# Optimization experiments

Measured on AMD Instinct MI355X. Metric: run time of the kernel, lower is better.

The kernel has to match this reference:

```python
import jax, jax.numpy as jnp
import numpy as np

B, SEQ, DIM, D, K = 32, 2048, 512, 512, 128


def _ln(x, g, b, eps=1e-5):
    m = x.mean(-1, keepdims=True)
    v = ((x - m) ** 2).mean(-1, keepdims=True)
    return (x - m) / jnp.sqrt(v + eps) * g + b


def _gelu(v):
    return jax.nn.gelu(v, approximate=False)


def _diff_topk(s, k, t):
    # s: (B, N) scores; iterative relaxed top-k (Xie & Ermon style).
    def step(carry, _):
        a = jax.nn.softmax(carry / t, axis=-1)
        carry = carry + jnp.log(jnp.clip(1.0 - a, 1e-6, 1.0))
        return carry, a
    _, Ws = jax.lax.scan(step, s, None, length=k)  # (k, B, N)
    return jnp.transpose(Ws, (1, 0, 2))            # (B, k, N)


def setup_inputs():
    key = jax.random.key(0)
    ks = jax.random.split(key, 6)
    w = lambda k_, shape: jax.random.normal(k_, shape, dtype=jnp.float32) * 0.02
    return {
        'x': jax.random.normal(ks[0], (B, SEQ, DIM), dtype=jnp.float32),
        'tau': jnp.array(0.0, dtype=jnp.float32),
        'ln1_g': jnp.ones((DIM,), jnp.float32), 'ln1_b': jnp.zeros((DIM,), jnp.float32),
        'W1': w(ks[1], (DIM, D)), 'b1': jnp.zeros((D,), jnp.float32),
        'ln2_g': jnp.ones((SEQ,), jnp.float32), 'ln2_b': jnp.zeros((SEQ,), jnp.float32),
        'W2': w(ks[2], (SEQ, SEQ)), 'b2': jnp.zeros((SEQ,), jnp.float32),
        'ln3_g': jnp.ones((D,), jnp.float32), 'ln3_b': jnp.zeros((D,), jnp.float32),
        'W3': w(ks[3], (D, D + 1)), 'b3': jnp.zeros((D + 1,), jnp.float32),
        'ln4_g': jnp.ones((D,), jnp.float32), 'ln4_b': jnp.zeros((D,), jnp.float32),
        'W4': w(ks[4], (D, DIM)), 'b4': jnp.zeros((DIM,), jnp.float32),
    }


def reference(x, tau, ln1_g, ln1_b, W1, b1, ln2_g, ln2_b, W2, b2,
              ln3_g, ln3_b, W3, b3, ln4_g, ln4_b, W4, b4):
    # tok_proj: LN(dim) -> Linear(dim, D) -> GELU
    x_tok = _gelu(_ln(x, ln1_g, ln1_b) @ W1 + b1)                  # (B, N, D)
    # ch_proj over the token axis: LN(seq) -> Linear(seq, seq) -> GELU
    xt = jnp.swapaxes(x_tok, 1, 2)                                  # (B, D, N)
    x_ch = jnp.swapaxes(_gelu(_ln(xt, ln2_g, ln2_b) @ W2 + b2), 1, 2)
    # proj -> split score | features
    h = _ln(x_tok + x_ch, ln3_g, ln3_b) @ W3 + b3                   # (B, N, D+1)
    x_score, x_proj = h[..., 0], h[..., 1:]
    t = jax.nn.sigmoid(jnp.clip(tau, -2.0, 5.0))
    Wmat = _diff_topk(x_score, K, t)                                # (B, k, N)
    Z = jnp.einsum('bkn,bnd->bkd', Wmat, x_proj)                    # soft gather
    Y = jnp.einsum('bkn,bkd->bnd', Wmat, Z)                         # soft scatter
    return _ln(x_proj + Y, ln4_g, ln4_b) @ W4 + b4                  # (B, N, dim)
```

## Files before the change

### kernel.cpp

```cpp
#include <hip/hip_runtime.h>
#include <math.h>

#define B_   32
#define SEQ_ 2048
#define DIM_ 512
#define KSEL 128

typedef _Float16 f16;
typedef _Float16 half8 __attribute__((ext_vector_type(8)));
typedef float floatx4 __attribute__((ext_vector_type(4)));

#define LSTR2 32

__device__ __forceinline__ float gelu_exact(float v) {
  return 0.5f * v * (1.0f + erff(v * 0.70710678118654752440f));
}

__global__ __launch_bounds__(256) void rowstats512(const float* __restrict__ X,
                                                   float* __restrict__ mean,
                                                   float* __restrict__ rstd) {
  int row = blockIdx.x * 4 + (threadIdx.x >> 6);
  int l = threadIdx.x & 63;
  const float4* p = (const float4*)(X + (size_t)row * 512);
  float4 v0 = p[l * 2], v1 = p[l * 2 + 1];
  float s = v0.x + v0.y + v0.z + v0.w + v1.x + v1.y + v1.z + v1.w;
  float q = v0.x*v0.x + v0.y*v0.y + v0.z*v0.z + v0.w*v0.w
          + v1.x*v1.x + v1.y*v1.y + v1.z*v1.z + v1.w*v1.w;
#pragma unroll
  for (int off = 32; off > 0; off >>= 1) {
    s += __shfl_down(s, off);
    q += __shfl_down(q, off);
  }
  if (l == 0) {
    float m = s * (1.0f / 512.0f);
    float var = q * (1.0f / 512.0f) - m * m;
    mean[row] = m;
    rstd[row] = rsqrtf(var + 1e-5f);
  }
}

__global__ __launch_bounds__(256) void rowstats512_f16(const f16* __restrict__ X,
                                                       float* __restrict__ mean,
                                                       float* __restrict__ rstd) {
  int row = blockIdx.x * 4 + (threadIdx.x >> 6);
  int l = threadIdx.x & 63;
  half8 h = *(const half8*)(X + (size_t)row * 512 + l * 8);
  float s = 0.f, q = 0.f;
#pragma unroll
  for (int i = 0; i < 8; ++i) { float v = (float)h[i]; s += v; q += v * v; }
#pragma unroll
  for (int off = 32; off > 0; off >>= 1) {
    s += __shfl_down(s, off);
    q += __shfl_down(q, off);
  }
  if (l == 0) {
    float m = s * (1.0f / 512.0f);
    float var = q * (1.0f / 512.0f) - m * m;
    mean[row] = m;
    rstd[row] = rsqrtf(var + 1e-5f);
  }
}

__global__ __launch_bounds__(512) void colstats_part(const f16* __restrict__ xtok,
                                                     float2* __restrict__ part) {
  int b = blockIdx.x >> 3, pr = blockIdx.x & 7;
  int d = threadIdx.x;
  const f16* src = xtok + ((size_t)b * SEQ_ + (size_t)pr * 256) * 512 + d;
  float s = 0.f, q = 0.f;
#pragma unroll 4
  for (int i = 0; i < 256; ++i) {
    float v = (float)src[(size_t)i * 512];
    s += v; q += v * v;
  }
  part[(size_t)blockIdx.x * 512 + d] = make_float2(s, q);
}

__global__ __launch_bounds__(256) void colstats_fin(const float2* __restrict__ part,
                                                    float* __restrict__ mean,
                                                    float* __restrict__ rstd) {
  int idx = blockIdx.x * 256 + threadIdx.x;
  int b = idx >> 9;
  float s = 0.f, q = 0.f;
#pragma unroll
  for (int p = 0; p < 8; ++p) {
    float2 v = part[((size_t)(b * 8 + p)) * 512 + (idx & 511)];
    s += v.x; q += v.y;
  }
  float m = s * (1.0f / 2048.0f);
  mean[idx] = m;
  rstd[idx] = rsqrtf(q * (1.0f / 2048.0f) - m * m + 1e-5f);
}

template <typename T>
__global__ __launch_bounds__(256) void transpose_cvt(const T* __restrict__ src,
                                                     f16* __restrict__ dst,
                                                     int R, int C, long sb, long db) {
  __shared__ float tile[32][33];
  const T* s = src + (long)blockIdx.z * sb;
  f16* d = dst + (long)blockIdx.z * db;
  int c0 = blockIdx.x * 32, r0 = blockIdx.y * 32;
  int tx = threadIdx.x, ty = threadIdx.y;
#pragma unroll
  for (int i = 0; i < 4; ++i) {
    int r = r0 + ty + i * 8, c = c0 + tx;
    if (r < R && c < C) tile[ty + i * 8][tx] = (float)s[(long)r * C + c];
  }
  __syncthreads();
#pragma unroll
  for (int i = 0; i < 4; ++i) {
    int c = c0 + ty + i * 8, r = r0 + tx;
    if (c < C && r < R) d[(long)c * R + r] = (f16)tile[tx][ty + i * 8];
  }
}

__global__ __launch_bounds__(256) void trans2_kernel(const f16* __restrict__ xtok,
    const float* __restrict__ mean2, const float* __restrict__ rstd2,
    const float* __restrict__ g2, const float* __restrict__ bl2,
    f16* __restrict__ A2) {
  __shared__ float tile[32][33];
  int b = blockIdx.z;
  const f16* src = xtok + (long)b * SEQ_ * 512;
  f16* dst = A2 + (long)b * 512 * SEQ_;
  int d0 = blockIdx.x * 32, s0 = blockIdx.y * 32;
  int tx = threadIdx.x, ty = threadIdx.y;
  float m = mean2[b * 512 + d0 + tx];
  float rs = rstd2[b * 512 + d0 + tx];
#pragma unroll
  for (int i = 0; i < 4; ++i) {
    int s = s0 + ty + i * 8;
    float v = (float)src[(long)s * 512 + d0 + tx];
    tile[ty + i * 8][tx] = (v - m) * rs * g2[s] + bl2[s];
  }
  __syncthreads();
#pragma unroll
  for (int i = 0; i < 4; ++i) {
    int d = d0 + ty + i * 8, s = s0 + tx;
    dst[(long)d * SEQ_ + s] = (f16)tile[tx][ty + i * 8];
  }
}


__device__ __forceinline__ void stage_gll(const f16* __restrict__ src, long ld,
                                          int row0, int k0, f16* S, int t) {
  int w = t >> 6, lane = t & 63;
  int r = lane >> 2, c8 = (lane & 3) * 8;
#pragma unroll
  for (int i = 0; i < 2; ++i) {
    int chunk = w * 2 + i;
    const f16* g = src + (long)(row0 + chunk * 16 + r) * ld + k0 + c8;
    f16* l = S + chunk * 16 * LSTR2;
    __builtin_amdgcn_global_load_lds(
        (const __attribute__((address_space(1))) void*)g,
        (__attribute__((address_space(3))) void*)l, 16, 0, 0);
  }
}

__device__ __forceinline__ void stage_a_ln_f32(const float* __restrict__ src, long ld,
    const float* __restrict__ mean, const float* __restrict__ rstd,
    const float* __restrict__ g, const float* __restrict__ bl,
    int row0, int k0, f16* S, int t) {
  int row = t >> 1, kc = (t & 1) * 16;
  int r = row0 + row, c = k0 + kc;
  float m = mean[r], sd = rstd[r];
  const float* p = src + (long)r * ld + c;
  float v[16], gv[16], bv[16];
#pragma unroll
  for (int i = 0; i < 4; ++i) {
    float4 q = ((const float4*)p)[i];
    v[i*4+0]=q.x; v[i*4+1]=q.y; v[i*4+2]=q.z; v[i*4+3]=q.w;
    float4 gq = ((const float4*)(g + c))[i];
    gv[i*4+0]=gq.x; gv[i*4+1]=gq.y; gv[i*4+2]=gq.z; gv[i*4+3]=gq.w;
    float4 bq = ((const float4*)(bl + c))[i];
    bv[i*4+0]=bq.x; bv[i*4+1]=bq.y; bv[i*4+2]=bq.z; bv[i*4+3]=bq.w;
  }
  half8 o0, o1;
#pragma unroll
  for (int i = 0; i < 8; ++i) {
    o0[i] = (f16)((v[i] - m) * sd * gv[i] + bv[i]);
    o1[i] = (f16)((v[i + 8] - m) * sd * gv[i + 8] + bv[i + 8]);
  }
  *(half8*)(S + row * LSTR2 + kc) = o0;
  *(half8*)(S + row * LSTR2 + kc + 8) = o1;
}

__device__ __forceinline__ void stage_a_ln_f16(const f16* __restrict__ src, long ld,
    const float* __restrict__ mean, const float* __restrict__ rstd,
    const float* __restrict__ g, const float* __restrict__ bl,
    int row0, int k0, f16* S, int t) {
  int row = t >> 1, kc = (t & 1) * 16;
  int r = row0 + row, c = k0 + kc;
  float m = mean[r], sd = rstd[r];
  const f16* p = src + (long)r * ld + c;
  half8 h0 = *(const half8*)(p);
  half8 h1 = *(const half8*)(p + 8);
  float gv[16], bv[16];
#pragma unroll
  for (int i = 0; i < 4; ++i) {
    float4 gq = ((const float4*)(g + c))[i];
    gv[i*4+0]=gq.x; gv[i*4+1]=gq.y; gv[i*4+2]=gq.z; gv[i*4+3]=gq.w;
    float4 bq = ((const float4*)(bl + c))[i];
    bv[i*4+0]=bq.x; bv[i*4+1]=bq.y; bv[i*4+2]=bq.z; bv[i*4+3]=bq.w;
  }
  half8 o0, o1;
#pragma unroll
  for (int i = 0; i < 8; ++i) {
    o0[i] = (f16)(((float)h0[i] - m) * sd * gv[i] + bv[i]);
    o1[i] = (f16)(((float)h1[i] - m) * sd * gv[i + 8] + bv[i + 8]);
  }
  *(half8*)(S + row * LSTR2 + kc) = o0;
  *(half8*)(S + row * LSTR2 + kc + 8) = o1;
}

__device__ __forceinline__ void mfma_step(const f16* As, const f16* Bs, int lane,
                                          int wr, int wc, floatx4 acc[4][4]) {
  int kc = (lane >> 4) * 8;
  int rl = lane & 15;
  half8 a[4], b[4];
#pragma unroll
  for (int mi = 0; mi < 4; ++mi)
    a[mi] = *(const half8*)(As + (wr * 64 + mi * 16 + rl) * LSTR2 + kc);
#pragma unroll
  for (int ni = 0; ni < 4; ++ni)
    b[ni] = *(const half8*)(Bs + (wc * 64 + ni * 16 + rl) * LSTR2 + kc);
#pragma unroll
  for (int mi = 0; mi < 4; ++mi)
#pragma unroll
    for (int ni = 0; ni < 4; ++ni)
      acc[mi][ni] = __builtin_amdgcn_mfma_f32_16x16x32_f16(a[mi], b[ni], acc[mi][ni], 0, 0, 0);
}

#define GEMM_PROLOG \
  __shared__ __attribute__((aligned(16))) f16 As[128 * LSTR2]; \
  __shared__ __attribute__((aligned(16))) f16 Bs[128 * LSTR2]; \
  int t = threadIdx.x; \
  int lane = t & 63, w = t >> 6, wr = w >> 1, wc = w & 1; \
  floatx4 acc[4][4]; \
  _Pragma("unroll") for (int mi = 0; mi < 4; ++mi) \
  _Pragma("unroll") for (int ni = 0; ni < 4; ++ni) acc[mi][ni] = (floatx4){0.f,0.f,0.f,0.f};

__global__ __launch_bounds__(256) void g1_kernel(const float* __restrict__ x,
    const float* __restrict__ mean, const float* __restrict__ rstd,
    const float* __restrict__ g1, const float* __restrict__ bl1,
    const f16* __restrict__ W1T, const float* __restrict__ b1,
    f16* __restrict__ xtok) {
  GEMM_PROLOG
  int m0 = blockIdx.y * 128, n0 = blockIdx.x * 128;
  for (int k0 = 0; k0 < 512; k0 += 32) {
    stage_a_ln_f32(x, 512, mean, rstd, g1, bl1, m0, k0, As, t);
    stage_gll(W1T, 512, n0, k0, Bs, t);
    __syncthreads();
    mfma_step(As, Bs, lane, wr, wc, acc);
    __syncthreads();
  }
#pragma unroll
  for (int mi = 0; mi < 4; ++mi)
#pragma unroll
    for (int ni = 0; ni < 4; ++ni) {
      int c = n0 + wc * 64 + ni * 16 + (lane & 15);
      float bias = b1[c];
      int r0 = m0 + wr * 64 + mi * 16 + (lane >> 4) * 4;
#pragma unroll
      for (int j = 0; j < 4; ++j)
        xtok[(long)(r0 + j) * 512 + c] = (f16)gelu_exact(acc[mi][ni][j] + bias);
    }
}

__global__ __launch_bounds__(256) void g2_kernel(const f16* __restrict__ W2T,
    const f16* __restrict__ A2, const float* __restrict__ b2,
    const f16* __restrict__ xtok, f16* __restrict__ xsum) {
  GEMM_PROLOG
  int b = blockIdx.z;
  int m0 = blockIdx.y * 128, n0 = blockIdx.x * 128;
  const f16* A2b = A2 + (long)b * 512 * SEQ_;
  const f16* xtb = xtok + (long)b * SEQ_ * 512;
  f16* xsb = xsum + (long)b * SEQ_ * 512;
  for (int k0 = 0; k0 < SEQ_; k0 += 32) {
    stage_gll(W2T, SEQ_, m0, k0, As, t);
    stage_gll(A2b, SEQ_, n0, k0, Bs, t);
    __syncthreads();
    mfma_step(As, Bs, lane, wr, wc, acc);
    __syncthreads();
  }
#pragma unroll
  for (int mi = 0; mi < 4; ++mi)
#pragma unroll
    for (int ni = 0; ni < 4; ++ni) {
      int c = n0 + wc * 64 + ni * 16 + (lane & 15);
      int r0 = m0 + wr * 64 + mi * 16 + (lane >> 4) * 4;
#pragma unroll
      for (int j = 0; j < 4; ++j) {
        int r = r0 + j;
        long idx = (long)r * 512 + c;
        float v = gelu_exact(acc[mi][ni][j] + b2[r]);
        xsb[idx] = (f16)((float)xtb[idx] + v);
      }
    }
}

__global__ __launch_bounds__(256) void g3_kernel(const f16* __restrict__ xsum,
    const float* __restrict__ mean, const float* __restrict__ rstd,
    const float* __restrict__ g3, const float* __restrict__ bl3,
    const f16* __restrict__ BT , const float* __restrict__ b3,
    f16* __restrict__ xproj) {
  GEMM_PROLOG
  int m0 = blockIdx.y * 128, n0 = blockIdx.x * 128;
  for (int k0 = 0; k0 < 512; k0 += 32) {
    stage_a_ln_f16(xsum, 512, mean, rstd, g3, bl3, m0, k0, As, t);
    stage_gll(BT, 512, n0, k0, Bs, t);
    __syncthreads();
    mfma_step(As, Bs, lane, wr, wc, acc);
    __syncthreads();
  }
#pragma unroll
  for (int mi = 0; mi < 4; ++mi)
#pragma unroll
    for (int ni = 0; ni < 4; ++ni) {
      int c = n0 + wc * 64 + ni * 16 + (lane & 15);
      float bias = b3[c + 1];
      int r0 = m0 + wr * 64 + mi * 16 + (lane >> 4) * 4;
#pragma unroll
      for (int j = 0; j < 4; ++j)
        xproj[(long)(r0 + j) * 512 + c] = (f16)(acc[mi][ni][j] + bias);
    }
}

__global__ __launch_bounds__(256) void score_kernel(const f16* __restrict__ xsum,
    const float* __restrict__ mean, const float* __restrict__ rstd,
    const float* __restrict__ g3, const float* __restrict__ bl3,
    const f16* __restrict__ w3c , const float* __restrict__ b3,
    float* __restrict__ xscore) {
  int row = blockIdx.x * 4 + (threadIdx.x >> 6);
  int l = threadIdx.x & 63;
  float m = mean[row], sd = rstd[row];
  half8 h = *(const half8*)(xsum + (long)row * 512 + l * 8);
  half8 wv = *(const half8*)(w3c + l * 8);
  float acc = 0.f;
#pragma unroll
  for (int i = 0; i < 8; ++i) {
    int d = l * 8 + i;
    float v = ((float)h[i] - m) * sd * g3[d] + bl3[d];
    acc += v * (float)wv[i];
  }
#pragma unroll
  for (int off = 32; off > 0; off >>= 1) acc += __shfl_down(acc, off);
  if (l == 0) xscore[row] = acc + b3[0];
}

__global__ __launch_bounds__(256) void topk_kernel(const float* __restrict__ xscore,
                                                   const float* __restrict__ tau,
                                                   f16* __restrict__ Wm) {
  int b = blockIdx.x, t = threadIdx.x;
  __shared__ float red[4];
  float tv = fminf(fmaxf(tau[0], -2.0f), 5.0f);
  float temp = 1.0f / (1.0f + expf(-tv));
  float it = 1.0f / temp;
  float c[8];
  const float* xs = xscore + (size_t)b * SEQ_;
#pragma unroll
  for (int i = 0; i < 8; ++i) c[i] = xs[t * 8 + i];
  for (int k = 0; k < KSEL; ++k) {
    float e[8];
    float p = 0.f;
#pragma unroll
    for (int i = 0; i < 8; ++i) { e[i] = expf(c[i] * it); p += e[i]; }
#pragma unroll
    for (int off = 32; off > 0; off >>= 1) p += __shfl_down(p, off);
    if ((t & 63) == 0) red[t >> 6] = p;
    __syncthreads();
    float S = red[0] + red[1] + red[2] + red[3];
    float iS = 1.0f / S;
    float a[8];
    half8 h;
#pragma unroll
    for (int i = 0; i < 8; ++i) { a[i] = e[i] * iS; h[i] = (f16)a[i]; }
    *(half8*)(Wm + ((size_t)b * KSEL + k) * SEQ_ + t * 8) = h;
#pragma unroll
    for (int i = 0; i < 8; ++i) c[i] += logf(fmaxf(1.0f - a[i], 1e-6f));
    __syncthreads();
  }
}

__global__ __launch_bounds__(256) void gz_kernel(const f16* __restrict__ Wm,
    const f16* __restrict__ xprojT, float* __restrict__ Zpart) {
  GEMM_PROLOG
  int b = blockIdx.z, kc = blockIdx.y;
  int n0 = blockIdx.x * 128;
  const f16* A = Wm + (long)b * KSEL * SEQ_;
  const f16* BT = xprojT + (long)b * 512 * SEQ_;
  float* Zb = Zpart + ((long)b * 2 + kc) * KSEL * 512;
  int kbeg = kc * 1024, kend = kbeg + 1024;
  for (int k0 = kbeg; k0 < kend; k0 += 32) {
    stage_gll(A, SEQ_, 0, k0, As, t);
    stage_gll(BT, SEQ_, n0, k0, Bs, t);
    __syncthreads();
    mfma_step(As, Bs, lane, wr, wc, acc);
    __syncthreads();
  }
#pragma unroll
  for (int mi = 0; mi < 4; ++mi)
#pragma unroll
    for (int ni = 0; ni < 4; ++ni) {
      int c = n0 + wc * 64 + ni * 16 + (lane & 15);
      int r0 = wr * 64 + mi * 16 + (lane >> 4) * 4;
#pragma unroll
      for (int j = 0; j < 4; ++j)
        Zb[(long)(r0 + j) * 512 + c] = acc[mi][ni][j];
    }
}

__global__ __launch_bounds__(256) void ztrans_kernel(const float* __restrict__ Zpart,
                                                     f16* __restrict__ ZT) {
  __shared__ float tile[32][33];
  int b = blockIdx.z;
  int c0 = blockIdx.x * 32, r0 = blockIdx.y * 32;
  int tx = threadIdx.x, ty = threadIdx.y;
  const float* p0 = Zpart + ((long)b * 2 + 0) * KSEL * 512;
  const float* p1 = Zpart + ((long)b * 2 + 1) * KSEL * 512;
#pragma unroll
  for (int i = 0; i < 4; ++i) {
    int r = r0 + ty + i * 8, c = c0 + tx;
    tile[ty + i * 8][tx] = p0[(long)r * 512 + c] + p1[(long)r * 512 + c];
  }
  __syncthreads();
  f16* d = ZT + (long)b * 512 * KSEL;
#pragma unroll
  for (int i = 0; i < 4; ++i) {
    int c = c0 + ty + i * 8, r = r0 + tx;
    d[(long)c * KSEL + r] = (f16)tile[tx][ty + i * 8];
  }
}

__global__ __launch_bounds__(256) void gy_kernel(const f16* __restrict__ WmT,
    const f16* __restrict__ ZT, const f16* __restrict__ xproj,
    f16* __restrict__ rbuf) {
  GEMM_PROLOG
  int b = blockIdx.z;
  int m0 = blockIdx.y * 128, n0 = blockIdx.x * 128;
  const f16* A = WmT + (long)b * SEQ_ * KSEL;
  const f16* BT = ZT + (long)b * 512 * KSEL;
  const f16* xpb = xproj + (long)b * SEQ_ * 512;
  f16* rb = rbuf + (long)b * SEQ_ * 512;
  for (int k0 = 0; k0 < KSEL; k0 += 32) {
    stage_gll(A, KSEL, m0, k0, As, t);
    stage_gll(BT, KSEL, n0, k0, Bs, t);
    __syncthreads();
    mfma_step(As, Bs, lane, wr, wc, acc);
    __syncthreads();
  }
#pragma unroll
  for (int mi = 0; mi < 4; ++mi)
#pragma unroll
    for (int ni = 0; ni < 4; ++ni) {
      int c = n0 + wc * 64 + ni * 16 + (lane & 15);
      int r0 = m0 + wr * 64 + mi * 16 + (lane >> 4) * 4;
#pragma unroll
      for (int j = 0; j < 4; ++j) {
        long idx = (long)(r0 + j) * 512 + c;
        rb[idx] = (f16)((float)xpb[idx] + acc[mi][ni][j]);
      }
    }
}

__global__ __launch_bounds__(256) void g4_kernel(const f16* __restrict__ rbuf,
    const float* __restrict__ mean, const float* __restrict__ rstd,
    const float* __restrict__ g4, const float* __restrict__ bl4,
    const f16* __restrict__ W4T, const float* __restrict__ b4,
    float* __restrict__ out) {
  GEMM_PROLOG
  int m0 = blockIdx.y * 128, n0 = blockIdx.x * 128;
  for (int k0 = 0; k0 < 512; k0 += 32) {
    stage_a_ln_f16(rbuf, 512, mean, rstd, g4, bl4, m0, k0, As, t);
    stage_gll(W4T, 512, n0, k0, Bs, t);
    __syncthreads();
    mfma_step(As, Bs, lane, wr, wc, acc);
    __syncthreads();
  }
#pragma unroll
  for (int mi = 0; mi < 4; ++mi)
#pragma unroll
    for (int ni = 0; ni < 4; ++ni) {
      int c = n0 + wc * 64 + ni * 16 + (lane & 15);
      float bias = b4[c];
      int r0 = m0 + wr * 64 + mi * 16 + (lane >> 4) * 4;
#pragma unroll
      for (int j = 0; j < 4; ++j)
        out[(long)(r0 + j) * 512 + c] = acc[mi][ni][j] + bias;
    }
}

extern "C" void kernel_launch(void* const* d_in, const int* in_sizes, int n_in,
                              void* d_out, int out_size, void* d_ws, size_t ws_size,
                              hipStream_t stream) {
  const float* x    = (const float*)d_in[0];
  const float* tau  = (const float*)d_in[1];
  const float* g1   = (const float*)d_in[2];
  const float* bl1  = (const float*)d_in[3];
  const float* W1   = (const float*)d_in[4];
  const float* b1   = (const float*)d_in[5];
  const float* g2   = (const float*)d_in[6];
  const float* bl2  = (const float*)d_in[7];
  const float* W2   = (const float*)d_in[8];
  const float* b2   = (const float*)d_in[9];
  const float* g3   = (const float*)d_in[10];
  const float* bl3  = (const float*)d_in[11];
  const float* W3   = (const float*)d_in[12];
  const float* b3   = (const float*)d_in[13];
  const float* g4   = (const float*)d_in[14];
  const float* bl4  = (const float*)d_in[15];
  const float* W4   = (const float*)d_in[16];
  const float* b4   = (const float*)d_in[17];
  float* out = (float*)d_out;

  const long NTOK = (long)B_ * SEQ_;

  char* ws = (char*)d_ws;
  f16* regA   = (f16*)(ws);
  f16* regB   = (f16*)(ws + (64l << 20));
  float* Zpart = (float*)(ws + (128l << 20));
  f16* W2T    = (f16*)(ws + (144l << 20));
  f16* W1T    = (f16*)(ws + (152l << 20));
  f16* W3T    = (f16*)(ws + (153l << 20));
  f16* W4T    = (f16*)(ws + (154l << 20));
  float* xscore = (float*)(ws + (155l << 20));
  float* meanA  = (float*)(ws + (156l << 20));
  float* rstdA  = meanA + NTOK;
  float* mean2  = rstdA + NTOK;
  float* rstd2  = mean2 + B_ * 512;
  float2* part  = (float2*)(rstd2 + B_ * 512);

  f16* xtok   = (f16*)d_out;
  f16* xprojT = (f16*)d_out;
  f16* Wm     = (f16*)((char*)d_out + (64l << 20));
  f16* WmT    = (f16*)((char*)d_out + (80l << 20));
  f16* ZT     = (f16*)((char*)d_out + (96l << 20));

  f16* A2    = regA;
  f16* xsum  = regB;
  f16* xproj = regA;
  f16* rbuf  = regB;

  dim3 tb(32, 8);

  transpose_cvt<float><<<dim3(16, 16, 1), tb, 0, stream>>>(W1, W1T, 512, 512, 0, 0);
  transpose_cvt<float><<<dim3(64, 64, 1), tb, 0, stream>>>(W2, W2T, 2048, 2048, 0, 0);
  transpose_cvt<float><<<dim3(17, 16, 1), tb, 0, stream>>>(W3, W3T, 512, 513, 0, 0);
  transpose_cvt<float><<<dim3(16, 16, 1), tb, 0, stream>>>(W4, W4T, 512, 512, 0, 0);

  rowstats512<<<NTOK / 4, 256, 0, stream>>>(x, meanA, rstdA);
  g1_kernel<<<dim3(4, 512), 256, 0, stream>>>(x, meanA, rstdA, g1, bl1, W1T, b1, xtok);

  colstats_part<<<B_ * 8, 512, 0, stream>>>(xtok, part);
  colstats_fin<<<64, 256, 0, stream>>>(part, mean2, rstd2);
  trans2_kernel<<<dim3(16, 64, B_), tb, 0, stream>>>(xtok, mean2, rstd2, g2, bl2, A2);
  g2_kernel<<<dim3(4, 16, B_), 256, 0, stream>>>(W2T, A2, b2, xtok, xsum);

  rowstats512_f16<<<NTOK / 4, 256, 0, stream>>>(xsum, meanA, rstdA);
  score_kernel<<<NTOK / 4, 256, 0, stream>>>(xsum, meanA, rstdA, g3, bl3, W3T, b3, xscore);
  g3_kernel<<<dim3(4, 512), 256, 0, stream>>>(xsum, meanA, rstdA, g3, bl3, W3T + 512, b3, xproj);

  topk_kernel<<<B_, 256, 0, stream>>>(xscore, tau, Wm);

  transpose_cvt<f16><<<dim3(16, 64, B_), tb, 0, stream>>>(xproj, xprojT, 2048, 512,
      (long)SEQ_ * 512, (long)512 * SEQ_);
  transpose_cvt<f16><<<dim3(64, 4, B_), tb, 0, stream>>>(Wm, WmT, 128, 2048,
      (long)KSEL * SEQ_, (long)SEQ_ * KSEL);

  gz_kernel<<<dim3(4, 2, B_), 256, 0, stream>>>(Wm, xprojT, Zpart);
  ztrans_kernel<<<dim3(16, 4, B_), tb, 0, stream>>>(Zpart, ZT);

  gy_kernel<<<dim3(4, 16, B_), 256, 0, stream>>>(WmT, ZT, xproj, rbuf);

  rowstats512_f16<<<NTOK / 4, 256, 0, stream>>>(rbuf, meanA, rstdA);
  g4_kernel<<<dim3(4, 512), 256, 0, stream>>>(rbuf, meanA, rstdA, g4, bl4, W4T, b4, out);
}
```

Measured before the change: 878.3 us.

## Rewrite ch-proj GEMM with 256x256 double-buffered swizzled LDS tiles and 8 waves

Replaces the 128x128, K=32, single-buffered g2 GEMM with a 512-thread kernel. Each block computes a 256x256 output tile over K=64 steps. Global-to-LDS loads are double-buffered and interleaved with the MFMA phases, use an XOR-swizzled LDS layout to avoid bank conflicts, and raise wave priority with s_setprio around MFMA bursts. This aims to cut global traffic per FLOP and hide load latency in the dominant SEQxSEQ GEMM. In exchange, the kernel uses 128 KB of LDS and many accumulator registers, which limits occupancy. The ZT buffer is also moved into the workspace.

```diff
diff --git a/kernel.cpp b/kernel.cpp
--- a/kernel.cpp
+++ b/kernel.cpp
@@ -139,7 +139,6 @@
   }
 }
 
-
 __device__ __forceinline__ void stage_gll(const f16* __restrict__ src, long ld,
                                           int row0, int k0, f16* S, int t) {
   int w = t >> 6, lane = t & 63;
@@ -265,36 +264,130 @@
     }
 }
 
-__global__ __launch_bounds__(256) void g2_kernel(const f16* __restrict__ W2T,
+__device__ __forceinline__ void stage_tile256(const f16* __restrict__ srcbase, long ld,
+                                              int k0, f16* dst, int tid) {
+  int w = tid >> 6, l = tid & 63;
+  int colh = ((l & 7) ^ (l >> 3)) << 3;
+  int rsub = w * 8 + (l >> 3);
+#pragma unroll
+  for (int q = 0; q < 4; ++q) {
+    const f16* g = srcbase + (long)(q * 64 + rsub) * ld + k0 + colh;
+    f16* lp = dst + (long)(q * 512 + w * 64) * 8;
+    __builtin_amdgcn_global_load_lds(
+        (const __attribute__((address_space(1))) void*)g,
+        (__attribute__((address_space(3))) void*)lp, 16, 0, 0);
+  }
+}
+
+__device__ __forceinline__ half8 frag_swz(const f16* buf, int row, int kslot, int rl) {
+  return *(const half8*)(buf + (long)row * 64 + (((kslot ^ (rl & 7))) << 3));
+}
+
+__global__ __launch_bounds__(512, 2) void g2_8p(const f16* __restrict__ W2T,
     const f16* __restrict__ A2, const float* __restrict__ b2,
     const f16* __restrict__ xtok, f16* __restrict__ xsum) {
-  GEMM_PROLOG
+  __shared__ __attribute__((aligned(16))) f16 Abuf[2][256 * 64];
+  __shared__ __attribute__((aligned(16))) f16 Bbuf[2][256 * 64];
+  int tid = threadIdx.x;
+  int l = tid & 63, w = tid >> 6;
+  int wr = w >> 2, wc = w & 3;
+  int rl = l & 15, sl = l >> 4;
   int b = blockIdx.z;
-  int m0 = blockIdx.y * 128, n0 = blockIdx.x * 128;
-  const f16* A2b = A2 + (long)b * 512 * SEQ_;
+  int m0 = blockIdx.y * 256;
+  int n0 = blockIdx.x * 256;
+  const f16* Am = W2T + (long)m0 * SEQ_;
+  const f16* Bm = A2 + (long)b * 512 * SEQ_ + (long)n0 * SEQ_;
   const f16* xtb = xtok + (long)b * SEQ_ * 512;
   f16* xsb = xsum + (long)b * SEQ_ * 512;
-  for (int k0 = 0; k0 < SEQ_; k0 += 32) {
-    stage_gll(W2T, SEQ_, m0, k0, As, t);
-    stage_gll(A2b, SEQ_, n0, k0, Bs, t);
-    __syncthreads();
-    mfma_step(As, Bs, lane, wr, wc, acc);
-    __syncthreads();
-  }
-#pragma unroll
-  for (int mi = 0; mi < 4; ++mi)
-#pragma unroll
-    for (int ni = 0; ni < 4; ++ni) {
-      int c = n0 + wc * 64 + ni * 16 + (lane & 15);
-      int r0 = m0 + wr * 64 + mi * 16 + (lane >> 4) * 4;
-#pragma unroll
-      for (int j = 0; j < 4; ++j) {
-        int r = r0 + j;
-        long idx = (long)r * 512 + c;
-        float v = gelu_exact(acc[mi][ni][j] + b2[r]);
-        xsb[idx] = (f16)((float)xtb[idx] + v);
+
+  floatx4 acc[8][4];
+#pragma unroll
+  for (int mf = 0; mf < 8; ++mf)
+#pragma unroll
+    for (int nf = 0; nf < 4; ++nf) acc[mf][nf] = (floatx4){0.f, 0.f, 0.f, 0.f};
+
+  const int NT = SEQ_ / 64;
+  stage_tile256(Am, SEQ_, 0, Abuf[0], tid);
+  stage_tile256(Bm, SEQ_, 0, Bbuf[0], tid);
+  __syncthreads();
+
+  for (int t = 0; t < NT; ++t) {
+    int c = t & 1;
+    const f16* Ab = Abuf[c];
+    const f16* Bb = Bbuf[c];
+    half8 afr[4], bfr[4];
+
+    if (t + 1 < NT) stage_tile256(Am, SEQ_, (t + 1) * 64, Abuf[c ^ 1], tid);
+#pragma unroll
+    for (int nf = 0; nf < 4; ++nf) bfr[nf] = frag_swz(Bb, wc * 64 + nf * 16 + rl, sl, rl);
+#pragma unroll
+    for (int mf = 0; mf < 4; ++mf) afr[mf] = frag_swz(Ab, wr * 128 + mf * 16 + rl, sl, rl);
+    __builtin_amdgcn_s_barrier();
+    __builtin_amdgcn_s_setprio(1);
+#pragma unroll
+    for (int mf = 0; mf < 4; ++mf)
+#pragma unroll
+      for (int nf = 0; nf < 4; ++nf)
+        acc[mf][nf] = __builtin_amdgcn_mfma_f32_16x16x32_f16(afr[mf], bfr[nf], acc[mf][nf], 0, 0, 0);
+    __builtin_amdgcn_s_setprio(0);
+    __builtin_amdgcn_s_barrier();
+
+    if (t + 1 < NT) stage_tile256(Bm, SEQ_, (t + 1) * 64, Bbuf[c ^ 1], tid);
+#pragma unroll
+    for (int mf = 0; mf < 4; ++mf) afr[mf] = frag_swz(Ab, wr * 128 + (mf + 4) * 16 + rl, sl, rl);
+    __builtin_amdgcn_s_barrier();
+    __builtin_amdgcn_s_setprio(1);
+#pragma unroll
+    for (int mf = 0; mf < 4; ++mf)
+#pragma unroll
+      for (int nf = 0; nf < 4; ++nf)
+        acc[mf + 4][nf] = __builtin_amdgcn_mfma_f32_16x16x32_f16(afr[mf], bfr[nf], acc[mf + 4][nf], 0, 0, 0);
+    __builtin_amdgcn_s_setprio(0);
+    __builtin_amdgcn_s_barrier();
+
+#pragma unroll
+    for (int nf = 0; nf < 4; ++nf) bfr[nf] = frag_swz(Bb, wc * 64 + nf * 16 + rl, 4 + sl, rl);
+#pragma unroll
+    for (int mf = 0; mf < 4; ++mf) afr[mf] = frag_swz(Ab, wr * 128 + mf * 16 + rl, 4 + sl, rl);
+    __builtin_amdgcn_s_barrier();
+    __builtin_amdgcn_s_setprio(1);
+#pragma unroll
+    for (int mf = 0; mf < 4; ++mf)
+#pragma unroll
+      for (int nf = 0; nf < 4; ++nf)
+        acc[mf][nf] = __builtin_amdgcn_mfma_f32_16x16x32_f16(afr[mf], bfr[nf], acc[mf][nf], 0, 0, 0);
+    __builtin_amdgcn_s_setprio(0);
+    __builtin_amdgcn_s_barrier();
+
+#pragma unroll
+    for (int mf = 0; mf < 4; ++mf) afr[mf] = frag_swz(Ab, wr * 128 + (mf + 4) * 16 + rl, 4 + sl, rl);
+    __builtin_amdgcn_s_setprio(1);
+#pragma unroll
+    for (int mf = 0; mf < 4; ++mf)
+#pragma unroll
+      for (int nf = 0; nf < 4; ++nf)
+        acc[mf + 4][nf] = __builtin_amdgcn_mfma_f32_16x16x32_f16(afr[mf], bfr[nf], acc[mf + 4][nf], 0, 0, 0);
+    __builtin_amdgcn_s_setprio(0);
+
+    __syncthreads();
+  }
+
+#pragma unroll
+  for (int mf = 0; mf < 8; ++mf) {
+    int rbase = m0 + wr * 128 + mf * 16 + sl * 4;
+#pragma unroll
+    for (int j = 0; j < 4; ++j) {
+      int r = rbase + j;
+      float bias = b2[r];
+      long rowoff = (long)r * 512;
+#pragma unroll
+      for (int nf = 0; nf < 4; ++nf) {
+        int cc = n0 + wc * 64 + nf * 16 + rl;
+        float v = gelu_exact(acc[mf][nf][j] + bias);
+        xsb[rowoff + cc] = (f16)((float)xtb[rowoff + cc] + v);
       }
     }
+  }
 }
 
 __global__ __launch_bounds__(256) void g3_kernel(const f16* __restrict__ xsum,
@@ -327,7 +420,7 @@
 __global__ __launch_bounds__(256) void score_kernel(const f16* __restrict__ xsum,
     const float* __restrict__ mean, const float* __restrict__ rstd,
     const float* __restrict__ g3, const float* __restrict__ bl3,
-    const f16* __restrict__ w3c , const float* __restrict__ b3,
+    const f16* __restrict__ w3c, const float* __restrict__ b3,
     float* __restrict__ xscore) {
   int row = blockIdx.x * 4 + (threadIdx.x >> 6);
   int l = threadIdx.x & 63;
@@ -527,12 +620,12 @@
   float* mean2  = rstdA + NTOK;
   float* rstd2  = mean2 + B_ * 512;
   float2* part  = (float2*)(rstd2 + B_ * 512);
+  f16* ZT     = (f16*)(ws + (157l << 20));
 
   f16* xtok   = (f16*)d_out;
   f16* xprojT = (f16*)d_out;
   f16* Wm     = (f16*)((char*)d_out + (64l << 20));
   f16* WmT    = (f16*)((char*)d_out + (80l << 20));
-  f16* ZT     = (f16*)((char*)d_out + (96l << 20));
 
   f16* A2    = regA;
   f16* xsum  = regB;
@@ -552,7 +645,7 @@
   colstats_part<<<B_ * 8, 512, 0, stream>>>(xtok, part);
   colstats_fin<<<64, 256, 0, stream>>>(part, mean2, rstd2);
   trans2_kernel<<<dim3(16, 64, B_), tb, 0, stream>>>(xtok, mean2, rstd2, g2, bl2, A2);
-  g2_kernel<<<dim3(4, 16, B_), 256, 0, stream>>>(W2T, A2, b2, xtok, xsum);
+  g2_8p<<<dim3(2, 8, B_), 512, 0, stream>>>(W2T, A2, b2, xtok, xsum);
 
   rowstats512_f16<<<NTOK / 4, 256, 0, stream>>>(xsum, meanA, rstdA);
   score_kernel<<<NTOK / 4, 256, 0, stream>>>(xsum, meanA, rstdA, g3, bl3, W3T, b3, xscore);
```

After: 889.1 us, median of 3. No clear change (+1.2%).

## Replace g2 GEMM with 256x256-tile, 8-wave, double-buffered pipelined kernel

Applied to the files above, without the earlier changes.

Replaces the 128x128 single-buffered g2 GEMM with a 256x256 tile kernel using 512 threads (8 waves), a double-buffered LDS pipeline of async global_load_lds stages interleaved with MFMA phases, and an XOR swizzle to avoid LDS bank conflicts. The goal is to overlap memory loads with 16x16x32 MFMA compute and raise arithmetic intensity for the largest GEMM. It also moves the ZT buffer into the workspace. The cost is heavier register pressure (128 accumulator floats per thread), manual barriers and vmcnt waits that are fragile if the tile count or staging order is wrong.

```diff
diff --git a/kernel.cpp b/kernel.cpp
--- a/kernel.cpp
+++ b/kernel.cpp
@@ -139,7 +139,6 @@
   }
 }
 
-
 __device__ __forceinline__ void stage_gll(const f16* __restrict__ src, long ld,
                                           int row0, int k0, f16* S, int t) {
   int w = t >> 6, lane = t & 63;
@@ -265,36 +264,124 @@
     }
 }
 
-__global__ __launch_bounds__(256) void g2_kernel(const f16* __restrict__ W2T,
+
+__device__ __forceinline__ void stage_half(const f16* __restrict__ srcbase, long ld,
+                                           f16* dst, int tid) {
+#pragma unroll
+  for (int q = 0; q < 2; ++q) {
+    int row = q * 128 + (tid >> 2);
+    int slot = (tid & 3) ^ ((row >> 1) & 3);
+    const f16* g = srcbase + (long)row * ld + slot * 8;
+    f16* lp = dst + (long)(q * 128 + (tid >> 6) * 16) * 32;
+    __builtin_amdgcn_global_load_lds(
+        (const __attribute__((address_space(1))) void*)g,
+        (__attribute__((address_space(3))) void*)lp, 16, 0, 0);
+  }
+}
+
+__device__ __forceinline__ half8 frag32(const f16* buf, int row, int sl) {
+  return *(const half8*)(buf + (long)row * 32 + ((sl ^ ((row >> 1) & 3)) << 3));
+}
+
+#define ASM_BAR()      asm volatile("s_barrier" ::: "memory")
+#define ASM_WAITBAR4() asm volatile("s_waitcnt vmcnt(4)\ns_barrier" ::: "memory")
+
+__global__ __launch_bounds__(512, 2) void g2_8p(const f16* __restrict__ W2T,
     const f16* __restrict__ A2, const float* __restrict__ b2,
     const f16* __restrict__ xtok, f16* __restrict__ xsum) {
-  GEMM_PROLOG
+  __shared__ __attribute__((aligned(16))) f16 Ah[2][2][256 * 32];
+  __shared__ __attribute__((aligned(16))) f16 Bh[2][2][256 * 32];
+  int tid = threadIdx.x;
+  int l = tid & 63, w = tid >> 6;
+  int wr = w >> 2, wc = w & 3;
+  int rl = l & 15, sl = l >> 4;
   int b = blockIdx.z;
-  int m0 = blockIdx.y * 128, n0 = blockIdx.x * 128;
-  const f16* A2b = A2 + (long)b * 512 * SEQ_;
+  int m0 = blockIdx.y * 256;
+  int n0 = blockIdx.x * 256;
+  const f16* Am = W2T + (long)m0 * SEQ_;
+  const f16* Bm = A2 + (long)b * 512 * SEQ_ + (long)n0 * SEQ_;
   const f16* xtb = xtok + (long)b * SEQ_ * 512;
   f16* xsb = xsum + (long)b * SEQ_ * 512;
-  for (int k0 = 0; k0 < SEQ_; k0 += 32) {
-    stage_gll(W2T, SEQ_, m0, k0, As, t);
-    stage_gll(A2b, SEQ_, n0, k0, Bs, t);
-    __syncthreads();
-    mfma_step(As, Bs, lane, wr, wc, acc);
-    __syncthreads();
-  }
-#pragma unroll
-  for (int mi = 0; mi < 4; ++mi)
-#pragma unroll
-    for (int ni = 0; ni < 4; ++ni) {
-      int c = n0 + wc * 64 + ni * 16 + (lane & 15);
-      int r0 = m0 + wr * 64 + mi * 16 + (lane >> 4) * 4;
-#pragma unroll
-      for (int j = 0; j < 4; ++j) {
-        int r = r0 + j;
-        long idx = (long)r * 512 + c;
-        float v = gelu_exact(acc[mi][ni][j] + b2[r]);
-        xsb[idx] = (f16)((float)xtb[idx] + v);
+
+  floatx4 acc[8][4];
+#pragma unroll
+  for (int mf = 0; mf < 8; ++mf)
+#pragma unroll
+    for (int nf = 0; nf < 4; ++nf) acc[mf][nf] = (floatx4){0.f, 0.f, 0.f, 0.f};
+
+  half8 afr[4], bfr[4];
+
+#define STAGE(base, tile, kk, dstbuf) \
+  stage_half(base + (long)((tile) & 31) * 64 + (kk) * 32, SEQ_, dstbuf, tid)
+
+#define READ_B(d, kk) \
+  _Pragma("unroll") for (int nf = 0; nf < 4; ++nf) \
+    bfr[nf] = frag32(Bh[d][kk], wc * 64 + nf * 16 + rl, sl);
+
+#define READ_A(d, kk, mb) \
+  _Pragma("unroll") for (int mi = 0; mi < 4; ++mi) \
+    afr[mi] = frag32(Ah[d][kk], wr * 128 + ((mb) + mi) * 16 + rl, sl);
+
+#define MFMA16(mb) \
+  __builtin_amdgcn_s_setprio(1); \
+  _Pragma("unroll") for (int mi = 0; mi < 4; ++mi) \
+  _Pragma("unroll") for (int nf = 0; nf < 4; ++nf) \
+    acc[(mb) + mi][nf] = __builtin_amdgcn_mfma_f32_16x16x32_f16(afr[mi], bfr[nf], acc[(mb) + mi][nf], 0, 0, 0); \
+  __builtin_amdgcn_s_setprio(0);
+
+  STAGE(Am, 0, 0, Ah[0][0]); STAGE(Am, 0, 1, Ah[0][1]);
+  STAGE(Bm, 0, 0, Bh[0][0]); STAGE(Bm, 0, 1, Bh[0][1]);
+  STAGE(Am, 1, 0, Ah[1][0]); STAGE(Bm, 1, 0, Bh[1][0]);
+  asm volatile("s_waitcnt vmcnt(0)" ::: "memory");
+  __builtin_amdgcn_s_barrier();
+
+  for (int i = 0; i < 16; ++i) {
+    STAGE(Am, 2 * i + 1, 1, Ah[1][1]);
+    READ_B(0, 0); READ_A(0, 0, 0);
+    ASM_BAR(); MFMA16(0); ASM_BAR();
+    STAGE(Bm, 2 * i + 1, 1, Bh[1][1]);
+    READ_A(0, 0, 4);
+    ASM_BAR(); MFMA16(4); ASM_BAR();
+    STAGE(Am, 2 * i + 2, 0, Ah[0][0]);
+    READ_B(0, 1); READ_A(0, 1, 0);
+    ASM_BAR(); MFMA16(0); ASM_BAR();
+    STAGE(Bm, 2 * i + 2, 0, Bh[0][0]);
+    READ_A(0, 1, 4);
+    ASM_BAR(); MFMA16(4); ASM_WAITBAR4();
+    STAGE(Am, 2 * i + 2, 1, Ah[0][1]);
+    READ_B(1, 0); READ_A(1, 0, 0);
+    ASM_BAR(); MFMA16(0); ASM_BAR();
+    STAGE(Bm, 2 * i + 2, 1, Bh[0][1]);
+    READ_A(1, 0, 4);
+    ASM_BAR(); MFMA16(4); ASM_BAR();
+    STAGE(Am, 2 * i + 3, 0, Ah[1][0]);
+    READ_B(1, 1); READ_A(1, 1, 0);
+    ASM_BAR(); MFMA16(0); ASM_BAR();
+    STAGE(Bm, 2 * i + 3, 0, Bh[1][0]);
+    READ_A(1, 1, 4);
+    ASM_BAR(); MFMA16(4); ASM_WAITBAR4();
+  }
+
+#pragma unroll
+  for (int mf = 0; mf < 8; ++mf) {
+    int rbase = m0 + wr * 128 + mf * 16 + sl * 4;
+#pragma unroll
+    for (int j = 0; j < 4; ++j) {
+      int r = rbase + j;
+      float bias = b2[r];
+      long rowoff = (long)r * 512;
+#pragma unroll
+      for (int nf = 0; nf < 4; ++nf) {
+        int cc = n0 + wc * 64 + nf * 16 + rl;
+        float v = gelu_exact(acc[mf][nf][j] + bias);
+        xsb[rowoff + cc] = (f16)((float)xtb[rowoff + cc] + v);
       }
     }
+  }
+#undef STAGE
+#undef READ_B
+#undef READ_A
+#undef MFMA16
 }
 
 __global__ __launch_bounds__(256) void g3_kernel(const f16* __restrict__ xsum,
@@ -327,7 +414,7 @@
 __global__ __launch_bounds__(256) void score_kernel(const f16* __restrict__ xsum,
     const float* __restrict__ mean, const float* __restrict__ rstd,
     const float* __restrict__ g3, const float* __restrict__ bl3,
-    const f16* __restrict__ w3c , const float* __restrict__ b3,
+    const f16* __restrict__ w3c, const float* __restrict__ b3,
     float* __restrict__ xscore) {
   int row = blockIdx.x * 4 + (threadIdx.x >> 6);
   int l = threadIdx.x & 63;
@@ -527,12 +614,12 @@
   float* mean2  = rstdA + NTOK;
   float* rstd2  = mean2 + B_ * 512;
   float2* part  = (float2*)(rstd2 + B_ * 512);
+  f16* ZT     = (f16*)(ws + (157l << 20));
 
   f16* xtok   = (f16*)d_out;
   f16* xprojT = (f16*)d_out;
   f16* Wm     = (f16*)((char*)d_out + (64l << 20));
   f16* WmT    = (f16*)((char*)d_out + (80l << 20));
-  f16* ZT     = (f16*)((char*)d_out + (96l << 20));
 
   f16* A2    = regA;
   f16* xsum  = regB;
@@ -552,7 +639,7 @@
   colstats_part<<<B_ * 8, 512, 0, stream>>>(xtok, part);
   colstats_fin<<<64, 256, 0, stream>>>(part, mean2, rstd2);
   trans2_kernel<<<dim3(16, 64, B_), tb, 0, stream>>>(xtok, mean2, rstd2, g2, bl2, A2);
-  g2_kernel<<<dim3(4, 16, B_), 256, 0, stream>>>(W2T, A2, b2, xtok, xsum);
+  g2_8p<<<dim3(2, 8, B_), 512, 0, stream>>>(W2T, A2, b2, xtok, xsum);
 
   rowstats512_f16<<<NTOK / 4, 256, 0, stream>>>(xsum, meanA, rstdA);
   score_kernel<<<NTOK / 4, 256, 0, stream>>>(xsum, meanA, rstdA, g3, bl3, W3T, b3, xscore);
```

After: 893.7 us. No clear change (+1.7%).
